# Kernel optimization log

Measured on AMD Instinct MI355X. Metric: run time of the kernel, lower is better.

The kernel has to match this reference:

```python
import jax, jax.numpy as jnp
import numpy as np

# Longformer-style attention: blocked sliding-window (radius W) + attention to
# the first G global tokens. Source class body was truncated, so this follows
# the canonical Longformer local+global formulation.
B, S, D = 2, 4096, 1024
H, DH = 16, 64          # num_heads, head_dim (H*DH == D)
W = 256                  # one-sided window radius == block size
G = 64                   # number of global tokens (prefix)


def setup_inputs() -> dict:
    key = jax.random.key(0)
    ks = jax.random.split(key, 5)
    x = jax.random.normal(ks[0], (B, S, D), jnp.float32)
    init = 0.02
    Wq = jax.random.normal(ks[1], (D, D), jnp.float32) * init
    Wk = jax.random.normal(ks[2], (D, D), jnp.float32) * init
    Wv = jax.random.normal(ks[3], (D, D), jnp.float32) * init
    Wo = jax.random.normal(ks[4], (D, D), jnp.float32) * init
    return {"x": x, "Wq": Wq, "Wk": Wk, "Wv": Wv, "Wo": Wo}


def _split_heads(t):
    # [B,S,D] -> [B,H,S,DH]
    return t.reshape(B, S, H, DH).transpose(0, 2, 1, 3)


def _local_mask():
    nb = S // W
    blk = jnp.arange(nb)[:, None, None]
    qi = jnp.arange(W)[None, :, None]
    kj = jnp.arange(3 * W)[None, None, :]
    i_abs = blk * W + qi                    # absolute query index
    j_abs = blk * W - W + kj                # absolute key index in 3-block strip
    return ((j_abs >= 0) & (j_abs < S) &
            (jnp.abs(j_abs - i_abs) <= W) &
            (j_abs >= G))                    # global keys handled separately


def reference(x, Wq, Wk, Wv, Wo):
    nb = S // W
    scale = 1.0 / np.sqrt(DH).astype(np.float32)
    q = _split_heads(x @ Wq)                 # [B,H,S,DH]
    k = _split_heads(x @ Wk)
    v = _split_heads(x @ Wv)

    qb = q.reshape(B, H, nb, W, DH)
    pad = ((0, 0), (0, 0), (1, 1), (0, 0), (0, 0))
    kp = jnp.pad(k.reshape(B, H, nb, W, DH), pad)
    vp = jnp.pad(v.reshape(B, H, nb, W, DH), pad)
    # 3-block strips: [B,H,nb,3W,DH]
    k3 = jnp.concatenate([kp[:, :, :-2], kp[:, :, 1:-1], kp[:, :, 2:]], axis=3)
    v3 = jnp.concatenate([vp[:, :, :-2], vp[:, :, 1:-1], vp[:, :, 2:]], axis=3)

    s_loc = jnp.einsum('bhnqd,bhnkd->bhnqk', qb, k3) * scale  # [B,H,nb,W,3W]
    s_loc = jnp.where(_local_mask()[None, None], s_loc, jnp.float32(-1e9))

    kg, vg = k[:, :, :G], v[:, :, :G]        # global prefix tokens
    s_glb = jnp.einsum('bhnqd,bhgd->bhnqg', qb, kg) * scale    # [B,H,nb,W,G]

    p = jax.nn.softmax(jnp.concatenate([s_loc, s_glb], axis=-1), axis=-1)
    p_loc, p_glb = p[..., :3 * W], p[..., 3 * W:]

    out = (jnp.einsum('bhnqk,bhnkd->bhnqd', p_loc, v3) +
           jnp.einsum('bhnqg,bhgd->bhnqd', p_glb, vg))         # [B,H,nb,W,DH]
    out = out.reshape(B, H, S, DH).transpose(0, 2, 1, 3).reshape(B, S, D)
    return out @ Wo
```

## Files before the change

### kernel.cpp

```cpp
#include <hip/hip_runtime.h>

#define BB   2
#define SS   4096
#define DD   1024
#define HH   16
#define DHH  64
#define WW   256
#define GG   64
#define NBLK 16

typedef unsigned short ushort_t;
typedef short  s16x8 __attribute__((ext_vector_type(8)));
typedef float  f32x4 __attribute__((ext_vector_type(4)));

#define QSCALE 0.18033688011112042f

__device__ __forceinline__ ushort_t f2b(float f) {
  unsigned int u = __builtin_bit_cast(unsigned int, f);
  unsigned int r = (u + 0x7fffu + ((u >> 16) & 1u)) >> 16;
  return (ushort_t)r;
}

__device__ __forceinline__ ushort_t f2b1(float f) {
  unsigned int r;
  asm("v_cvt_pk_bf16_f32 %0, %1, %2" : "=v"(r) : "v"(f), "v"(f));
  return (ushort_t)r;
}

__device__ __forceinline__ float exp2f_fast(float x) {
  return __builtin_amdgcn_exp2f(x);
}

__device__ __forceinline__ void gld16(const void* g, void* l) {
  __builtin_amdgcn_global_load_lds(
      (const __attribute__((address_space(1))) void*)g,
      (__attribute__((address_space(3))) void*)l, 16, 0, 0);
}

__global__ __launch_bounds__(256) void xcast(
    const float* __restrict__ x, ushort_t* __restrict__ xb) {
  size_t i = ((size_t)blockIdx.x * 256 + threadIdx.x) * 8;
  float4 f0 = *(const float4*)&x[i];
  float4 f1 = *(const float4*)&x[i + 4];
  ushort_t t[8];
  t[0] = f2b(f0.x); t[1] = f2b(f0.y); t[2] = f2b(f0.z); t[3] = f2b(f0.w);
  t[4] = f2b(f1.x); t[5] = f2b(f1.y); t[6] = f2b(f1.z); t[7] = f2b(f1.w);
  *(uint4*)&xb[i] = *(const uint4*)t;
}

__global__ __launch_bounds__(256) void transpose_w(
    const float* __restrict__ Wq, const float* __restrict__ Wk,
    const float* __restrict__ Wv, const float* __restrict__ Wo,
    ushort_t* __restrict__ outBase) {
  const float* src = (blockIdx.z == 0) ? Wq : (blockIdx.z == 1) ? Wk
                    : (blockIdx.z == 2) ? Wv : Wo;
  ushort_t* dst = outBase + (size_t)blockIdx.z * (1024 * 1024);
  __shared__ __align__(16) ushort_t t[64][72];
  const int tid = threadIdx.x;
  const int bx = blockIdx.x * 64, by = blockIdx.y * 64;
  const int c4 = (tid & 15) * 4;
  const int r16 = tid >> 4;
  for (int rr = r16; rr < 64; rr += 16) {
    float4 f = *(const float4*)&src[(size_t)(by + rr) * 1024 + bx + c4];
    t[c4 + 0][rr] = f2b(f.x);
    t[c4 + 1][rr] = f2b(f.y);
    t[c4 + 2][rr] = f2b(f.z);
    t[c4 + 3][rr] = f2b(f.w);
  }
  __syncthreads();
  const int sr = tid >> 3;
  const int sc = (tid & 7) * 8;
  for (int rr = sr; rr < 64; rr += 32) {
    *(uint4*)&dst[(size_t)(bx + rr) * 1024 + by + sc] = *(const uint4*)&t[rr][sc];
  }
}

template <int MODE>
__global__ __launch_bounds__(256) void gemm_bt(
    const ushort_t* __restrict__ A, const ushort_t* __restrict__ Bt,
    ushort_t* __restrict__ O0, ushort_t* __restrict__ O1,
    ushort_t* __restrict__ O2, float* __restrict__ Of, int K) {
  __shared__ __align__(16) ushort_t As[128 * 64];
  __shared__ __align__(16) ushort_t Bs[128 * 64];
  const int tid  = threadIdx.x;
  const int lane = tid & 63;
  const int w    = tid >> 6;
  const int quad = lane >> 4;
  const int l16  = lane & 15;
  const int bm = blockIdx.x * 128;
  const int bn = blockIdx.y * 128;
  const int sr = tid >> 3;
  const int sc = (tid & 7) * 8;
  const int wm = (w & 1) * 64;
  const int wn = (w >> 1) * 64;

  f32x4 acc[4][4] = {};

  for (int k0 = 0; k0 < K; k0 += 64) {
    __syncthreads();
#pragma unroll
    for (int cpy = 0; cpy < 4; cpy++) {
      int r = sr + cpy * 32;
      gld16(&A[(size_t)(bm + r) * K + k0 + sc], &As[r * 64 + sc]);
      gld16(&Bt[(size_t)(bn + r) * K + k0 + sc], &Bs[r * 64 + sc]);
    }
    __syncthreads();
#pragma unroll
    for (int kk = 0; kk < 64; kk += 32) {
      s16x8 a[4], b[4];
#pragma unroll
      for (int t = 0; t < 4; t++)
        a[t] = *(const s16x8*)&As[(wm + t * 16 + l16) * 64 + kk + quad * 8];
#pragma unroll
      for (int t = 0; t < 4; t++)
        b[t] = *(const s16x8*)&Bs[(wn + t * 16 + l16) * 64 + kk + quad * 8];
#pragma unroll
      for (int i = 0; i < 4; i++)
#pragma unroll
        for (int j = 0; j < 4; j++)
          acc[i][j] = __builtin_amdgcn_mfma_f32_16x16x32_bf16(a[i], b[j], acc[i][j], 0, 0, 0);
    }
  }

#pragma unroll
  for (int i = 0; i < 4; i++) {
#pragma unroll
    for (int j = 0; j < 4; j++) {
#pragma unroll
      for (int r = 0; r < 4; r++) {
        int m = bm + wm + i * 16 + quad * 4 + r;
        int n = bn + wn + j * 16 + l16;
        float av = acc[i][j][r];
        if (MODE == 0) {
          int n1 = n & 1023;
          int h = n1 >> 6, dh = n1 & 63;
          int b = m >> 12, s = m & 4095;
          if (n < 1024) {
            O0[(((size_t)b * HH + h) * SS + s) * DHH + dh] = f2b(av * QSCALE);
          } else if (n < 2048) {
            O1[(((size_t)b * HH + h) * SS + s) * DHH + dh] = f2b(av);
          } else {
            O2[(((size_t)b * HH + h) * DHH + dh) * SS + s] = f2b(av);
          }
        } else {
          Of[(size_t)m * DD + n] = av;
        }
      }
    }
  }
}

__global__ __launch_bounds__(256, 2) void attn_kernel(
    const ushort_t* __restrict__ q, const ushort_t* __restrict__ k,
    const ushort_t* __restrict__ vT, ushort_t* __restrict__ out) {
  const int blk = blockIdx.x;
  const int h   = blockIdx.y;
  const int b   = blockIdx.z;
  const int tid  = threadIdx.x;
  const int lane = tid & 63;
  const int w    = tid >> 6;
  const int quad = lane >> 4;
  const int l16  = lane & 15;

  const size_t bh = ((size_t)b * HH + h) * SS * DHH;
  const ushort_t* qb  = q + bh;
  const ushort_t* kb  = k + bh;
  const ushort_t* vtb = vT + bh;

  __shared__ __align__(16) ushort_t Ps[4][64 * 64];
  ushort_t* Pw = &Ps[w][0];

  const int q0 = blk * WW + w * 64;

  const int wbase = ((l16 >> 3) << 9) + (quad << 5) + (l16 & 7);
  const int rbase = (quad << 9) + (l16 << 3);

  s16x8 aq[4][2];
#pragma unroll
  for (int mt = 0; mt < 4; mt++)
#pragma unroll
    for (int x = 0; x < 2; x++)
      aq[mt][x] = *(const s16x8*)&qb[(size_t)(q0 + mt * 16 + l16) * DHH + x * 32 + quad * 8];

  f32x4 oacc[4][4] = {};
  f32x4 rsacc[4] = {};

  s16x8 vone;
#pragma unroll
  for (int j = 0; j < 8; j++) vone[j] = (short)0x3F80;

  s16x8 bk[4][2];
  s16x8 bv[4][2];

  auto LOADK = [&](int j0s) {
    const ushort_t* kc = kb + (size_t)j0s * DHH;
#pragma unroll
    for (int nt = 0; nt < 4; nt++)
#pragma unroll
      for (int x = 0; x < 2; x++)
        bk[nt][x] = *(const s16x8*)&kc[(nt * 16 + l16) * DHH + x * 32 + quad * 8];
  };
  auto LOADV = [&](int j0s) {
    const ushort_t* vc = vtb + j0s;
#pragma unroll
    for (int dt = 0; dt < 4; dt++)
#pragma unroll
      for (int x = 0; x < 2; x++)
        bv[dt][x] = *(const s16x8*)&vc[(size_t)(dt * 16 + l16) * SS + x * 32 + quad * 8];
  };

  const int jlo = (q0 - (int)WW < (int)GG) ? (int)GG : (q0 - (int)WW);
  int jhi = q0 + (int)WW;
  if (jhi > SS - 64) jhi = SS - 64;

  int j0  = jlo;
  int j0u = __builtin_amdgcn_readfirstlane(j0);
  LOADK(j0u);

  bool last = false;
  while (!last) {
    int jn = j0 + 64;
    if (j0 == 0) { last = true; jn = 0; }
    else if (jn > jhi) jn = 0;

    LOADV(j0u);

    const int dlt = j0 - q0;
    const bool needmask = (j0 != 0) && (dlt < -193 || dlt > 193);

#pragma unroll
    for (int nt = 0; nt < 4; nt++) {
      const int j = j0 + nt * 16 + l16;
#pragma unroll
      for (int mt = 0; mt < 4; mt++) {
        f32x4 s4 = {0.f, 0.f, 0.f, 0.f};
        s4 = __builtin_amdgcn_mfma_f32_16x16x32_bf16(aq[mt][0], bk[nt][0], s4, 0, 0, 0);
        s4 = __builtin_amdgcn_mfma_f32_16x16x32_bf16(aq[mt][1], bk[nt][1], s4, 0, 0, 0);
#pragma unroll
        for (int r = 0; r < 4; r++) {
          float p;
          if (needmask) {
            int i = q0 + mt * 16 + quad * 4 + r;
            int d = j - i;
            p = (d <= (int)WW && d >= -(int)WW) ? exp2f_fast(s4[r]) : 0.0f;
          } else {
            p = exp2f_fast(s4[r]);
          }
          Pw[wbase + nt * 1024 + mt * 128 + r * 8] = f2b1(p);
        }
      }
    }

    int jnu = __builtin_amdgcn_readfirstlane(jn);
    if (!last) LOADK(jnu);

    __builtin_amdgcn_s_setprio(1);
#pragma unroll
    for (int ll = 0; ll < 64; ll += 32) {
      s16x8 ap[4];
#pragma unroll
      for (int mt = 0; mt < 4; mt++)
        ap[mt] = *(const s16x8*)&Pw[rbase + (ll >> 3) * 512 + mt * 128];
#pragma unroll
      for (int mt = 0; mt < 4; mt++) {
        rsacc[mt] = __builtin_amdgcn_mfma_f32_16x16x32_bf16(ap[mt], vone, rsacc[mt], 0, 0, 0);
#pragma unroll
        for (int dt = 0; dt < 4; dt++)
          oacc[mt][dt] = __builtin_amdgcn_mfma_f32_16x16x32_bf16(ap[mt], bv[dt][ll >> 5], oacc[mt][dt], 0, 0, 0);
      }
    }
    __builtin_amdgcn_s_setprio(0);

    j0 = jn; j0u = jnu;
  }

#pragma unroll
  for (int mt = 0; mt < 4; mt++) {
#pragma unroll
    for (int r = 0; r < 4; r++) {
      float inv = __builtin_amdgcn_rcpf(rsacc[mt][r]);
      int srow2 = q0 + mt * 16 + quad * 4 + r;
      size_t orow = ((size_t)b * SS + srow2) * DD + h * DHH;
#pragma unroll
      for (int dt = 0; dt < 4; dt++)
        out[orow + dt * 16 + l16] = f2b1(oacc[mt][dt][r] * inv);
    }
  }
}

extern "C" void kernel_launch(void* const* d_in, const int* in_sizes, int n_in,
                              void* d_out, int out_size, void* d_ws, size_t ws_size,
                              hipStream_t stream) {
  const float *x, *Wq, *Wk, *Wv, *Wo;
  if (n_in == 5 && in_sizes[4] == 8388608) {
    Wk = (const float*)d_in[0]; Wo = (const float*)d_in[1];
    Wq = (const float*)d_in[2]; Wv = (const float*)d_in[3];
    x  = (const float*)d_in[4];
  } else {
    x  = (const float*)d_in[0]; Wq = (const float*)d_in[1];
    Wk = (const float*)d_in[2]; Wv = (const float*)d_in[3];
    Wo = (const float*)d_in[4];
  }
  float* out = (float*)d_out;

  char* ws = (char*)d_ws;
  ushort_t* wqkvT = (ushort_t*)(ws);
  ushort_t* woT   = (ushort_t*)(ws + 6291456);
  ushort_t* qbuf  = (ushort_t*)(ws + 8388608);
  ushort_t* kbuf  = (ushort_t*)(ws + 8388608 + 16777216);
  ushort_t* vbuf  = (ushort_t*)(ws + 8388608 + 2 * 16777216);
  ushort_t* attn  = (ushort_t*)(ws + 8388608 + 3 * 16777216);
  ushort_t* xb    = attn;

  xcast<<<dim3(4096), 256, 0, stream>>>(x, xb);
  transpose_w<<<dim3(16, 16, 4), 256, 0, stream>>>(Wq, Wk, Wv, Wo, wqkvT);
  gemm_bt<0><<<dim3(64, 24), 256, 0, stream>>>(xb, wqkvT, qbuf, kbuf, vbuf, nullptr, 1024);
  attn_kernel<<<dim3(NBLK, HH, BB), 256, 0, stream>>>(qbuf, kbuf, vbuf, attn);
  gemm_bt<1><<<dim3(64, 8), 256, 0, stream>>>(attn, woT, nullptr, nullptr, nullptr, out, 1024);
}
```

Baseline: 268.6 us.

## Replace GEMM with 256x256-tile, 8-wave, double-buffered, swizzled-LDS pipelined kernel

Rewrites the projection GEMM to use 256x256 output tiles with 512 threads, double-buffered LDS split into K-halves, and an XOR swizzle on LDS chunks to avoid bank conflicts. Global loads for future K-tiles are issued between MFMA phases with explicit vmcnt/lgkmcnt waits, raw barriers and setprio, so memory traffic overlaps compute. The larger tiles cut global reloads per output. The trade-off is far fewer blocks (384 and 128), which may underfill the GPU's CUs, plus heavier register pressure from 128 accumulators.

```diff
diff --git a/kernel.cpp b/kernel.cpp
--- a/kernel.cpp
+++ b/kernel.cpp
@@ -76,60 +76,120 @@
 }
 
 template <int MODE>
-__global__ __launch_bounds__(256) void gemm_bt(
+__global__ __launch_bounds__(512, 2) void gemm256(
     const ushort_t* __restrict__ A, const ushort_t* __restrict__ Bt,
     ushort_t* __restrict__ O0, ushort_t* __restrict__ O1,
     ushort_t* __restrict__ O2, float* __restrict__ Of, int K) {
-  __shared__ __align__(16) ushort_t As[128 * 64];
-  __shared__ __align__(16) ushort_t Bs[128 * 64];
+  __shared__ __align__(16) ushort_t As[2][2][256 * 32];
+  __shared__ __align__(16) ushort_t Bs[2][2][256 * 32];
+
   const int tid  = threadIdx.x;
   const int lane = tid & 63;
   const int w    = tid >> 6;
   const int quad = lane >> 4;
   const int l16  = lane & 15;
-  const int bm = blockIdx.x * 128;
-  const int bn = blockIdx.y * 128;
-  const int sr = tid >> 3;
-  const int sc = (tid & 7) * 8;
-  const int wm = (w & 1) * 64;
-  const int wn = (w >> 1) * 64;
-
-  f32x4 acc[4][4] = {};
-
-  for (int k0 = 0; k0 < K; k0 += 64) {
-    __syncthreads();
-#pragma unroll
-    for (int cpy = 0; cpy < 4; cpy++) {
-      int r = sr + cpy * 32;
-      gld16(&A[(size_t)(bm + r) * K + k0 + sc], &As[r * 64 + sc]);
-      gld16(&Bt[(size_t)(bn + r) * K + k0 + sc], &Bs[r * 64 + sc]);
-    }
-    __syncthreads();
-#pragma unroll
-    for (int kk = 0; kk < 64; kk += 32) {
-      s16x8 a[4], b[4];
-#pragma unroll
-      for (int t = 0; t < 4; t++)
-        a[t] = *(const s16x8*)&As[(wm + t * 16 + l16) * 64 + kk + quad * 8];
-#pragma unroll
-      for (int t = 0; t < 4; t++)
-        b[t] = *(const s16x8*)&Bs[(wn + t * 16 + l16) * 64 + kk + quad * 8];
-#pragma unroll
-      for (int i = 0; i < 4; i++)
-#pragma unroll
-        for (int j = 0; j < 4; j++)
-          acc[i][j] = __builtin_amdgcn_mfma_f32_16x16x32_bf16(a[i], b[j], acc[i][j], 0, 0, 0);
-    }
-  }
-
-#pragma unroll
-  for (int i = 0; i < 4; i++) {
+  const int wr   = w >> 2;
+  const int wc   = w & 3;
+  const int bm   = blockIdx.x * 256;
+  const int bn   = blockIdx.y * 256;
+
+  const int srow = tid >> 2;
+  const int sch  = (tid & 3) ^ ((srow >> 1) & 3);
+  const ushort_t* Ag = A + (size_t)(bm + srow) * K + sch * 8;
+  const ushort_t* Bg = Bt + (size_t)(bn + srow) * K + sch * 8;
+
+  const int chofs = ((quad ^ ((l16 >> 1) & 3)) << 3);
+
+  auto stage = [&](ushort_t* slab, const ushort_t* g) {
+    gld16(g, &slab[tid * 8]);
+    gld16(g + (size_t)128 * K, &slab[4096 + tid * 8]);
+  };
+
+  f32x4 acc[8][4] = {};
+  s16x8 afrag[4], bfrag[4];
+
+  auto ldA = [&](int buf, int kkh, int i) {
+    const int row = wr * 128 + i * 16 + l16;
+    return *(const s16x8*)&As[buf][kkh][row * 32 + chofs];
+  };
+  auto ldB = [&](int buf, int kkh, int j) {
+    const int row = wc * 64 + j * 16 + l16;
+    return *(const s16x8*)&Bs[buf][kkh][row * 32 + chofs];
+  };
+  auto mfma16 = [&](int ih) {
+    __builtin_amdgcn_s_setprio(1);
+#pragma unroll
+    for (int t = 0; t < 4; t++)
+#pragma unroll
+      for (int j = 0; j < 4; j++)
+        acc[ih * 4 + t][j] = __builtin_amdgcn_mfma_f32_16x16x32_bf16(
+            afrag[t], bfrag[j], acc[ih * 4 + t][j], 0, 0, 0);
+    __builtin_amdgcn_s_setprio(0);
+  };
+
+  const int NT = K >> 6;
+
+  stage(&Bs[0][0][0], Bg);
+  stage(&As[0][0][0], Ag);
+  stage(&Bs[0][1][0], Bg + 32);
+  stage(&As[0][1][0], Ag + 32);
+  asm volatile("s_waitcnt vmcnt(4)" ::: "memory");
+  stage(&Bs[1][0][0], Bg + 64);
+  stage(&As[1][0][0], Ag + 64);
+  stage(&Bs[1][1][0], Bg + 96);
+  asm volatile("s_waitcnt vmcnt(6)" ::: "memory");
+  __builtin_amdgcn_s_barrier();
+
+#pragma unroll 1
+  for (int kt = 0; kt < NT; ++kt) {
+    const int buf = kt & 1;
+#pragma unroll
+    for (int j = 0; j < 4; j++) bfrag[j] = ldB(buf, 0, j);
+#pragma unroll
+    for (int t = 0; t < 4; t++) afrag[t] = ldA(buf, 0, t);
+    if (kt + 1 < NT) stage(&As[buf ^ 1][1][0], Ag + (size_t)(kt + 1) * 64 + 32);
+    __builtin_amdgcn_s_barrier();
+    asm volatile("s_waitcnt lgkmcnt(0)" ::: "memory");
+    mfma16(0);
+    __builtin_amdgcn_s_barrier();
+#pragma unroll
+    for (int t = 0; t < 4; t++) afrag[t] = ldA(buf, 0, 4 + t);
+    if (kt + 2 < NT) stage(&Bs[buf][0][0], Bg + (size_t)(kt + 2) * 64);
+    __builtin_amdgcn_s_barrier();
+    asm volatile("s_waitcnt lgkmcnt(0)" ::: "memory");
+    mfma16(1);
+    __builtin_amdgcn_s_barrier();
+#pragma unroll
+    for (int j = 0; j < 4; j++) bfrag[j] = ldB(buf, 1, j);
+#pragma unroll
+    for (int t = 0; t < 4; t++) afrag[t] = ldA(buf, 1, t);
+    if (kt + 2 < NT) stage(&As[buf][0][0], Ag + (size_t)(kt + 2) * 64);
+    __builtin_amdgcn_s_barrier();
+    asm volatile("s_waitcnt lgkmcnt(0)" ::: "memory");
+    mfma16(0);
+    __builtin_amdgcn_s_barrier();
+#pragma unroll
+    for (int t = 0; t < 4; t++) afrag[t] = ldA(buf, 1, 4 + t);
+    if (kt + 2 < NT) {
+      stage(&Bs[buf][1][0], Bg + (size_t)(kt + 2) * 64 + 32);
+      asm volatile("s_waitcnt vmcnt(6)" ::: "memory");
+    } else if (kt + 1 < NT) {
+      asm volatile("s_waitcnt vmcnt(0)" ::: "memory");
+    }
+    __builtin_amdgcn_s_barrier();
+    asm volatile("s_waitcnt lgkmcnt(0)" ::: "memory");
+    mfma16(1);
+    __builtin_amdgcn_s_barrier();
+  }
+
+#pragma unroll
+  for (int i = 0; i < 8; i++) {
 #pragma unroll
     for (int j = 0; j < 4; j++) {
 #pragma unroll
       for (int r = 0; r < 4; r++) {
-        int m = bm + wm + i * 16 + quad * 4 + r;
-        int n = bn + wn + j * 16 + l16;
+        int m = bm + wr * 128 + i * 16 + quad * 4 + r;
+        int n = bn + wc * 64 + j * 16 + l16;
         float av = acc[i][j][r];
         if (MODE == 0) {
           int n1 = n & 1023;
@@ -314,7 +374,7 @@
 
   xcast<<<dim3(4096), 256, 0, stream>>>(x, xb);
   transpose_w<<<dim3(16, 16, 4), 256, 0, stream>>>(Wq, Wk, Wv, Wo, wqkvT);
-  gemm_bt<0><<<dim3(64, 24), 256, 0, stream>>>(xb, wqkvT, qbuf, kbuf, vbuf, nullptr, 1024);
+  gemm256<0><<<dim3(32, 12), 512, 0, stream>>>(xb, wqkvT, qbuf, kbuf, vbuf, nullptr, 1024);
   attn_kernel<<<dim3(NBLK, HH, BB), 256, 0, stream>>>(qbuf, kbuf, vbuf, attn);
-  gemm_bt<1><<<dim3(64, 8), 256, 0, stream>>>(attn, woT, nullptr, nullptr, nullptr, out, 1024);
-}
+  gemm256<1><<<dim3(32, 4), 512, 0, stream>>>(attn, woT, nullptr, nullptr, nullptr, out, 1024);
+}
```

Result: no change. 272.7 us (+1.6%).

## Rewrite projection GEMMs with 4-stage async LDS pipeline, swizzle, larger tiles, XCD mapping

Applied to the files above, without the earlier changes.

Replaces the single-buffered GEMM with a 512-thread kernel that keeps a 4-slot ring of 32-wide K slabs in LDS. It prefetches three stages ahead using manual vmcnt waits and raw barriers, and XOR-swizzles LDS chunk placement to avoid bank conflicts. Tiles are widened to 128x384 for the QKV projection and 128x256 for the output projection, and block IDs are remapped so neighbouring tiles share an XCD. The goal is to hide global-load latency and raise MFMA utilisation, at the cost of more LDS, more registers and fragile hand-tuned wait counts.

```diff
diff --git a/kernel.cpp b/kernel.cpp
--- a/kernel.cpp
+++ b/kernel.cpp
@@ -14,6 +14,8 @@
 typedef float  f32x4 __attribute__((ext_vector_type(4)));
 
 #define QSCALE 0.18033688011112042f
+
+#define VMCNT(n) asm volatile("s_waitcnt vmcnt(" #n ")" ::: "memory")
 
 __device__ __forceinline__ ushort_t f2b(float f) {
   unsigned int u = __builtin_bit_cast(unsigned int, f);
@@ -75,61 +77,104 @@
   }
 }
 
-template <int MODE>
-__global__ __launch_bounds__(256) void gemm_bt(
+template <int MODE, int WN>
+__global__ __launch_bounds__(512, 2) void gemmk(
     const ushort_t* __restrict__ A, const ushort_t* __restrict__ Bt,
     ushort_t* __restrict__ O0, ushort_t* __restrict__ O1,
     ushort_t* __restrict__ O2, float* __restrict__ Of, int K) {
-  __shared__ __align__(16) ushort_t As[128 * 64];
-  __shared__ __align__(16) ushort_t Bs[128 * 64];
+  constexpr int BN    = WN * 64;
+  constexpr int LB    = BN / 128;
+  constexpr int ASLAB = 128 * 32;
+  constexpr int BSLAB = BN * 32;
+  __shared__ __align__(16) ushort_t SH[4 * ASLAB + 4 * BSLAB];
+
   const int tid  = threadIdx.x;
   const int lane = tid & 63;
   const int w    = tid >> 6;
   const int quad = lane >> 4;
   const int l16  = lane & 15;
-  const int bm = blockIdx.x * 128;
-  const int bn = blockIdx.y * 128;
-  const int sr = tid >> 3;
-  const int sc = (tid & 7) * 8;
-  const int wm = (w & 1) * 64;
-  const int wn = (w >> 1) * 64;
-
-  f32x4 acc[4][4] = {};
-
-  for (int k0 = 0; k0 < K; k0 += 64) {
-    __syncthreads();
-#pragma unroll
-    for (int cpy = 0; cpy < 4; cpy++) {
-      int r = sr + cpy * 32;
-      gld16(&A[(size_t)(bm + r) * K + k0 + sc], &As[r * 64 + sc]);
-      gld16(&Bt[(size_t)(bn + r) * K + k0 + sc], &Bs[r * 64 + sc]);
-    }
-    __syncthreads();
-#pragma unroll
-    for (int kk = 0; kk < 64; kk += 32) {
-      s16x8 a[4], b[4];
-#pragma unroll
-      for (int t = 0; t < 4; t++)
-        a[t] = *(const s16x8*)&As[(wm + t * 16 + l16) * 64 + kk + quad * 8];
-#pragma unroll
-      for (int t = 0; t < 4; t++)
-        b[t] = *(const s16x8*)&Bs[(wn + t * 16 + l16) * 64 + kk + quad * 8];
-#pragma unroll
-      for (int i = 0; i < 4; i++)
-#pragma unroll
-        for (int j = 0; j < 4; j++)
-          acc[i][j] = __builtin_amdgcn_mfma_f32_16x16x32_bf16(a[i], b[j], acc[i][j], 0, 0, 0);
-    }
+  const int wr   = w >> 2;
+  const int wc   = w & 3;
+
+  const int id  = blockIdx.x + (gridDim.x * blockIdx.y);
+  const int xcd = id & 7;
+  const int seq = id >> 3;
+  const int nx  = (xcd << 3) + (seq & 7);
+  const int ny  = seq >> 3;
+  const int bm  = nx * 128;
+  const int bn  = ny * BN;
+
+  const int srow = tid >> 2;
+  const int sch  = (tid & 3) ^ ((srow >> 1) & 3);
+  const ushort_t* Ag = A + (size_t)(bm + srow) * K + sch * 8;
+  const ushort_t* Bg = Bt + (size_t)(bn + srow) * K + sch * 8;
+
+  const int chofs = ((quad ^ ((l16 >> 1) & 3)) << 3);
+
+  f32x4 acc[4][WN] = {};
+
+  const int NT = K >> 5;
+
+#pragma unroll
+  for (int s0 = 0; s0 < 3; s0++) {
+    gld16(Ag + (size_t)s0 * 32, &SH[s0 * ASLAB + tid * 8]);
+#pragma unroll
+    for (int p = 0; p < LB; p++)
+      gld16(Bg + (size_t)(p * 128) * K + (size_t)s0 * 32,
+            &SH[4 * ASLAB + s0 * BSLAB + p * 4096 + tid * 8]);
+  }
+  if constexpr (WN == 6) VMCNT(8); else VMCNT(6);
+  __builtin_amdgcn_s_barrier();
+
+#pragma unroll 1
+  for (int s = 0; s < NT; ++s) {
+    const int buf = s & 3;
+    const ushort_t* Ab = &SH[buf * ASLAB];
+    const ushort_t* Bb = &SH[4 * ASLAB + buf * BSLAB];
+    s16x8 afrag[4], bfrag[WN];
+#pragma unroll
+    for (int j = 0; j < WN; j++)
+      bfrag[j] = *(const s16x8*)&Bb[(wc * (WN * 16) + j * 16 + l16) * 32 + chofs];
+#pragma unroll
+    for (int t = 0; t < 4; t++)
+      afrag[t] = *(const s16x8*)&Ab[(wr * 64 + t * 16 + l16) * 32 + chofs];
+
+    if (s + 3 < NT) {
+      const int sn = s + 3;
+      ushort_t* An = &SH[(sn & 3) * ASLAB];
+      ushort_t* Bn = &SH[4 * ASLAB + (sn & 3) * BSLAB];
+      gld16(Ag + (size_t)sn * 32, &An[tid * 8]);
+#pragma unroll
+      for (int p = 0; p < LB; p++)
+        gld16(Bg + (size_t)(p * 128) * K + (size_t)sn * 32,
+              &Bn[p * 4096 + tid * 8]);
+      if constexpr (WN == 6) VMCNT(8); else VMCNT(6);
+    } else if (s + 3 == NT) {
+      if constexpr (WN == 6) VMCNT(4); else VMCNT(3);
+    } else if (s + 2 == NT) {
+      VMCNT(0);
+    }
+    __builtin_amdgcn_s_barrier();
+    asm volatile("s_waitcnt lgkmcnt(0)" ::: "memory");
+    __builtin_amdgcn_s_setprio(1);
+#pragma unroll
+    for (int t = 0; t < 4; t++)
+#pragma unroll
+      for (int j = 0; j < WN; j++)
+        acc[t][j] = __builtin_amdgcn_mfma_f32_16x16x32_bf16(
+            afrag[t], bfrag[j], acc[t][j], 0, 0, 0);
+    __builtin_amdgcn_s_setprio(0);
+    __builtin_amdgcn_s_barrier();
   }
 
 #pragma unroll
   for (int i = 0; i < 4; i++) {
 #pragma unroll
-    for (int j = 0; j < 4; j++) {
+    for (int j = 0; j < WN; j++) {
 #pragma unroll
       for (int r = 0; r < 4; r++) {
-        int m = bm + wm + i * 16 + quad * 4 + r;
-        int n = bn + wn + j * 16 + l16;
+        int m = bm + wr * 64 + i * 16 + quad * 4 + r;
+        int n = bn + wc * (WN * 16) + j * 16 + l16;
         float av = acc[i][j][r];
         if (MODE == 0) {
           int n1 = n & 1023;
@@ -314,7 +359,7 @@
 
   xcast<<<dim3(4096), 256, 0, stream>>>(x, xb);
   transpose_w<<<dim3(16, 16, 4), 256, 0, stream>>>(Wq, Wk, Wv, Wo, wqkvT);
-  gemm_bt<0><<<dim3(64, 24), 256, 0, stream>>>(xb, wqkvT, qbuf, kbuf, vbuf, nullptr, 1024);
+  gemmk<0, 6><<<dim3(64, 8), 512, 0, stream>>>(xb, wqkvT, qbuf, kbuf, vbuf, nullptr, 1024);
   attn_kernel<<<dim3(NBLK, HH, BB), 256, 0, stream>>>(qbuf, kbuf, vbuf, attn);
-  gemm_bt<1><<<dim3(64, 8), 256, 0, stream>>>(attn, woT, nullptr, nullptr, nullptr, out, 1024);
-}
+  gemmk<1, 4><<<dim3(64, 4), 512, 0, stream>>>(attn, woT, nullptr, nullptr, nullptr, out, 1024);
+}
```

Result: faster. 245.8 us (-8.5%).
